# Kernel tuning notes

Hardware: AMD Instinct MI355X
Metric: run time of the kernel (lower is better)

The kernel has to match this reference:

```python
import jax, jax.numpy as jnp
import numpy as np

N = 100000      # nodes
E = 1600000     # edges (avg degree 16)
D_IN, D_H, D_OUT = 100, 256, 47
EPS = 1e-5


def setup_inputs() -> dict:
    key = jax.random.key(0)
    ks = jax.random.split(key, 10)
    w = lambda k, s: jax.random.normal(k, s, jnp.float32) * 0.02
    return {
        "x": jax.random.normal(ks[0], (N, D_IN), jnp.float32),
        "edge_index": jax.random.randint(ks[1], (2, E), 0, N),
        # SAGEConv 0: lin_l (aggregated neighbors, has bias), lin_r (root, no bias)
        "wl0": w(ks[2], (D_IN, D_H)), "wr0": w(ks[3], (D_IN, D_H)), "b0": jnp.zeros((D_H,), jnp.float32),
        "g0": jnp.ones((D_H,), jnp.float32), "be0": jnp.zeros((D_H,), jnp.float32),
        # SAGEConv 1
        "wl1": w(ks[4], (D_H, D_H)), "wr1": w(ks[5], (D_H, D_H)), "b1": jnp.zeros((D_H,), jnp.float32),
        "g1": jnp.ones((D_H,), jnp.float32), "be1": jnp.zeros((D_H,), jnp.float32),
        # SAGEConv 2 (output)
        "wl2": w(ks[6], (D_H, D_OUT)), "wr2": w(ks[7], (D_H, D_OUT)), "b2": jnp.zeros((D_OUT,), jnp.float32),
    }


def _sage_conv(x, src, dst, wl, wr, b):
    # mean aggregation of source-node features onto destination nodes
    agg = jax.ops.segment_sum(x[src], dst, num_segments=N)          # [N, d_in]
    cnt = jax.ops.segment_sum(jnp.ones((src.shape[0],), x.dtype), dst, num_segments=N)
    mean = agg / jnp.maximum(cnt, 1.0)[:, None]                     # 0 in-degree -> 0
    return mean @ wl + x @ wr + b


def _bn(h, gamma, beta):
    m = h.mean(axis=0)
    v = h.var(axis=0)
    return (h - m) * jax.lax.rsqrt(v + EPS) * gamma + beta


def reference(x, edge_index, wl0, wr0, b0, g0, be0, wl1, wr1, b1, g1, be1, wl2, wr2, b2):
    src, dst = edge_index[0], edge_index[1]
    h = jax.nn.relu(_bn(_sage_conv(x, src, dst, wl0, wr0, b0), g0, be0))
    h = jax.nn.relu(_bn(_sage_conv(h, src, dst, wl1, wr1, b1), g1, be1))
    h = _sage_conv(h, src, dst, wl2, wr2, b2)
    return jax.nn.log_softmax(h, axis=1)
```

## Files before the change

kernel.cpp:

```cpp
#include <hip/hip_runtime.h>
#include <hip/hip_bf16.h>
#include <math.h>

#define DEVFN __device__ __forceinline__

typedef unsigned int uint32;
typedef unsigned short ushort_t;

using bf16x8 = __attribute__((ext_vector_type(8))) short;
using f32x4  = __attribute__((ext_vector_type(4))) float;

DEVFN float bf2f(ushort_t u) {
    union { uint32 i; float f; } v; v.i = ((uint32)u) << 16; return v.f;
}
DEVFN ushort_t f2bf(float f) {
    union { float f; uint32 i; } v; v.f = f;
    uint32 u = v.i;
    uint32 r = (u + 0x7FFFu + ((u >> 16) & 1u)) >> 16;
    return (ushort_t)r;
}

DEVFN void gload_lds16(const void* g, void* l) {
    __builtin_amdgcn_global_load_lds(
        (const __attribute__((address_space(1))) void*)g,
        (__attribute__((address_space(3))) void*)l, 16, 0, 0);
}

__global__ void k_cast_x(const float* __restrict__ x, ushort_t* __restrict__ xb, int N) {
    int total = N * 128;
    for (int i = blockIdx.x * blockDim.x + threadIdx.x; i < total; i += gridDim.x * blockDim.x) {
        int col = i & 127, row = i >> 7;
        float v = (col < 100) ? x[row * 100 + col] : 0.f;
        xb[i] = f2bf(v);
    }
}

__global__ void k_cast_w(const float* __restrict__ w, ushort_t* __restrict__ wt,
                         int K, int Nout, int Kp, int Np) {
    int total = Np * Kp;
    for (int i = blockIdx.x * blockDim.x + threadIdx.x; i < total; i += gridDim.x * blockDim.x) {
        int k = i % Kp, n = i / Kp;
        float v = (k < K && n < Nout) ? w[k * Nout + n] : 0.f;
        wt[i] = f2bf(v);
    }
}

__global__ void k_bincount(const int* __restrict__ dst, int E, int CH, int nbins, int nblk,
                           int* __restrict__ binCnt) {
    __shared__ int scnt[128];
    int blk = blockIdx.x, tid = threadIdx.x;
    for (int b = tid; b < 128; b += 256) scnt[b] = 0;
    __syncthreads();
    int e0 = blk * CH, e1 = min(E, e0 + CH);
    for (int i = e0 + tid; i < e1; i += 256)
        atomicAdd(&scnt[dst[i] >> 10], 1);
    __syncthreads();
    for (int b = tid; b < nbins; b += 256) binCnt[b * nblk + blk] = scnt[b];
}

__global__ void k_blocksum(const int* __restrict__ v, int n, int* __restrict__ bsum) {
    __shared__ int s[1024];
    int i = blockIdx.x * 1024 + threadIdx.x;
    s[threadIdx.x] = (i < n) ? v[i] : 0;
    __syncthreads();
    for (int o = 512; o > 0; o >>= 1) {
        if (threadIdx.x < o) s[threadIdx.x] += s[threadIdx.x + o];
        __syncthreads();
    }
    if (threadIdx.x == 0) bsum[blockIdx.x] = s[0];
}

__global__ void k_scanb(int* __restrict__ bsum, int NB) {
    if (blockIdx.x == 0 && threadIdx.x == 0) {
        int acc = 0;
        for (int i = 0; i < NB; ++i) { int v = bsum[i]; bsum[i] = acc; acc += v; }
    }
}

__global__ void k_exscan(const int* __restrict__ v, const int* __restrict__ bsum,
                         int n, int* __restrict__ outOff) {
    __shared__ int s[1024];
    int t = threadIdx.x;
    int i = blockIdx.x * 1024 + t;
    int val = (i < n) ? v[i] : 0;
    s[t] = val;
    __syncthreads();
    for (int o = 1; o < 1024; o <<= 1) {
        int add = (t >= o) ? s[t - o] : 0;
        __syncthreads();
        s[t] += add;
        __syncthreads();
    }
    if (i < n) outOff[i] = s[t] - val + bsum[blockIdx.x];
}

__global__ void k_binscatter(const int* __restrict__ src, const int* __restrict__ dst,
                             int E, int CH, int nbins, int nblk,
                             const int* __restrict__ binOff, int* __restrict__ ebin) {
    __shared__ int scur[128];
    int blk = blockIdx.x, tid = threadIdx.x;
    for (int b = tid; b < nbins; b += 256) scur[b] = binOff[b * nblk + blk];
    __syncthreads();
    int e0 = blk * CH, e1 = min(E, e0 + CH);
    for (int i = e0 + tid; i < e1; i += 256) {
        int d = dst[i];
        int b = d >> 10;
        int pos = atomicAdd(&scur[b], 1);
        ebin[pos] = (src[i] << 10) | (d & 1023);
    }
}

__global__ void k_bincsr(const int* __restrict__ ebin, const int* __restrict__ binOff,
                         int E, int N, int nbins, int nblk,
                         int* __restrict__ offs, int* __restrict__ deg, int* __restrict__ csr) {
    __shared__ int sdeg[1024];
    __shared__ int scur[1024];
    int bin = blockIdx.x, t = threadIdx.x;
    int binStart = binOff[bin * nblk];
    int binEnd = (bin + 1 < nbins) ? binOff[(bin + 1) * nblk] : E;
    sdeg[t] = 0;
    __syncthreads();
    for (int i = binStart + t; i < binEnd; i += 1024)
        atomicAdd(&sdeg[ebin[i] & 1023], 1);
    __syncthreads();
    int v = sdeg[t];
    for (int o = 1; o < 1024; o <<= 1) {
        int add = (t >= o) ? sdeg[t - o] : 0;
        __syncthreads();
        sdeg[t] += add;
        __syncthreads();
    }
    int ex = sdeg[t] - v;
    int node = bin * 1024 + t;
    if (node < N) { offs[node] = binStart + ex; deg[node] = v; }
    scur[t] = ex;
    __syncthreads();
    for (int i = binStart + t; i < binEnd; i += 1024) {
        int e = ebin[i];
        int slot = atomicAdd(&scur[e & 1023], 1);
        csr[binStart + slot] = e >> 10;
    }
}

template <int DIMS>
__global__ void k_agg(const ushort_t* __restrict__ h, const int* __restrict__ offs,
                      const int* __restrict__ deg, const int* __restrict__ csr,
                      int N, ushort_t* __restrict__ mean) {
    constexpr int VPL = DIMS / 64;
    int wid = (blockIdx.x * blockDim.x + threadIdx.x) >> 6;
    int lane = threadIdx.x & 63;
    if (wid >= N) return;
    int off = offs[wid], cnt = deg[wid];
    float acc[VPL] = {};
    const ushort_t* hp = h + (size_t)lane * VPL;
    int j = 0;
    if constexpr (VPL == 2) {
        for (; j + 8 <= cnt; j += 8) {
            int s[8];
#pragma unroll
            for (int u = 0; u < 8; ++u) s[u] = csr[off + j + u];
            uint32 d[8];
#pragma unroll
            for (int u = 0; u < 8; ++u) d[u] = *(const uint32*)(hp + (size_t)s[u] * DIMS);
#pragma unroll
            for (int u = 0; u < 8; ++u) {
                acc[0] += bf2f((ushort_t)(d[u] & 0xffff));
                acc[1] += bf2f((ushort_t)(d[u] >> 16));
            }
        }
        for (; j < cnt; ++j) {
            uint32 u = *(const uint32*)(hp + (size_t)csr[off + j] * DIMS);
            acc[0] += bf2f((ushort_t)(u & 0xffff));
            acc[1] += bf2f((ushort_t)(u >> 16));
        }
    } else {
        for (; j + 8 <= cnt; j += 8) {
            int s[8];
#pragma unroll
            for (int u = 0; u < 8; ++u) s[u] = csr[off + j + u];
            uint2 d[8];
#pragma unroll
            for (int u = 0; u < 8; ++u) d[u] = *(const uint2*)(hp + (size_t)s[u] * DIMS);
#pragma unroll
            for (int u = 0; u < 8; ++u) {
                acc[0] += bf2f((ushort_t)(d[u].x & 0xffff));
                acc[1] += bf2f((ushort_t)(d[u].x >> 16));
                acc[2] += bf2f((ushort_t)(d[u].y & 0xffff));
                acc[3] += bf2f((ushort_t)(d[u].y >> 16));
            }
        }
        for (; j < cnt; ++j) {
            uint2 u = *(const uint2*)(hp + (size_t)csr[off + j] * DIMS);
            acc[0] += bf2f((ushort_t)(u.x & 0xffff));
            acc[1] += bf2f((ushort_t)(u.x >> 16));
            acc[2] += bf2f((ushort_t)(u.y & 0xffff));
            acc[3] += bf2f((ushort_t)(u.y >> 16));
        }
    }
    float inv = 1.f / fmaxf((float)cnt, 1.f);
    if constexpr (VPL == 2) {
        uint32 o = (uint32)f2bf(acc[0] * inv) | ((uint32)f2bf(acc[1] * inv) << 16);
        *(uint32*)(mean + (size_t)wid * DIMS + lane * 2) = o;
    } else {
        uint2 o;
        o.x = (uint32)f2bf(acc[0] * inv) | ((uint32)f2bf(acc[1] * inv) << 16);
        o.y = (uint32)f2bf(acc[2] * inv) | ((uint32)f2bf(acc[3] * inv) << 16);
        *(uint2*)(mean + (size_t)wid * DIMS + lane * 4) = o;
    }
}

template <int BN, int WAVES_N, int WM, int WN, int MODE>
__global__ __launch_bounds__(256) void k_gemm(
    const ushort_t* __restrict__ A1, const ushort_t* __restrict__ B1,
    const ushort_t* __restrict__ A2, const ushort_t* __restrict__ B2,
    int KP, const float* __restrict__ bias,
    ushort_t* __restrict__ out_bf, float* __restrict__ out_f,
    float* __restrict__ stats, int M) {
    constexpr int BM = 128, BK = 32;
    constexpr int M_REP = WM / 16, N_REP = WN / 16;
    constexpr int SIDES = (MODE == 0) ? 2 : 1;
    __shared__ ushort_t Alds[BM * BK];
    __shared__ ushort_t Blds[BN * BK];
    __shared__ float sstat[2][BN];
    const int tid = threadIdx.x, lane = tid & 63, wid = tid >> 6;
    const int wm = wid / WAVES_N, wn = wid % WAVES_N;
    const int row0 = blockIdx.x * BM, col0 = blockIdx.y * BN;
    if (MODE == 0) {
        for (int i = tid; i < 2 * BN; i += 256) (&sstat[0][0])[i] = 0.f;
    }
    f32x4 acc[M_REP][N_REP] = {};
    for (int side = 0; side < SIDES; ++side) {
        const ushort_t* A = side ? A2 : A1;
        const ushort_t* B = side ? B2 : B1;
        for (int kt = 0; kt < KP; kt += BK) {
            __syncthreads();
            for (int i = tid; i < BM * 4; i += 256) {
                int r = i >> 2, c = i & 3;
                int gr = row0 + r;
                if (gr >= M) gr = M - 1;
                gload_lds16(A + (size_t)gr * KP + kt + c * 8, Alds + i * 8);
            }
            for (int i = tid; i < BN * 4; i += 256) {
                int r = i >> 2, c = i & 3;
                gload_lds16(B + (size_t)(col0 + r) * KP + kt + c * 8, Blds + i * 8);
            }
            __syncthreads();
            bf16x8 a[M_REP], b[N_REP];
#pragma unroll
            for (int m = 0; m < M_REP; ++m)
                a[m] = *(const bf16x8*)&Alds[(wm * WM + m * 16 + (lane & 15)) * BK + (lane >> 4) * 8];
#pragma unroll
            for (int n = 0; n < N_REP; ++n)
                b[n] = *(const bf16x8*)&Blds[(wn * WN + n * 16 + (lane & 15)) * BK + (lane >> 4) * 8];
#pragma unroll
            for (int m = 0; m < M_REP; ++m)
#pragma unroll
                for (int n = 0; n < N_REP; ++n)
                    acc[m][n] = __builtin_amdgcn_mfma_f32_16x16x32_bf16(a[m], b[n], acc[m][n], 0, 0, 0);
        }
    }
#pragma unroll
    for (int n = 0; n < N_REP; ++n) {
        int lcol = wn * WN + n * 16 + (lane & 15);
        float s = 0.f, q = 0.f;
#pragma unroll
        for (int m = 0; m < M_REP; ++m) {
#pragma unroll
            for (int r = 0; r < 4; ++r) {
                int row = row0 + wm * WM + m * 16 + (lane >> 4) * 4 + r;
                float v = acc[m][n][r];
                if (row < M) {
                    if (MODE == 0) {
                        out_bf[(size_t)row * 256 + col0 + lcol] = f2bf(v);
                        s += v;
                        q += v * v;
                    } else {
                        if (lcol < 64) {
                            out_bf[(size_t)row * 64 + lcol] = f2bf(v);
                        } else {
                            int c = lcol - 64;
                            float bv = (c < 47) ? bias[c] : 0.f;
                            out_f[(size_t)row * 64 + c] = v + bv;
                        }
                    }
                }
            }
        }
        if (MODE == 0) {
            s += __shfl_xor(s, 16); s += __shfl_xor(s, 32);
            q += __shfl_xor(q, 16); q += __shfl_xor(q, 32);
            if (lane < 16) {
                atomicAdd(&sstat[0][lcol], s);
                atomicAdd(&sstat[1][lcol], q);
            }
        }
    }
    if (MODE == 0) {
        __syncthreads();
        for (int i = tid; i < BN; i += 256) {
            atomicAdd(&stats[col0 + i], sstat[0][i]);
            atomicAdd(&stats[256 + col0 + i], sstat[1][i]);
        }
    }
}

__global__ void k_bnrelu(const ushort_t* __restrict__ h, const float* __restrict__ stats,
                         const float* __restrict__ g, const float* __restrict__ be,
                         int M, ushort_t* __restrict__ out) {
    int c = threadIdx.x;
    float invM = 1.f / (float)M;
    float mean = stats[c] * invM;
    float var = stats[256 + c] * invM - mean * mean;
    float sc = g[c] * rsqrtf(var + 1e-5f);
    float sh = be[c] - mean * sc;
    for (int r = blockIdx.x; r < M; r += gridDim.x) {
        float v = bf2f(h[(size_t)r * 256 + c]) * sc + sh;
        out[(size_t)r * 256 + c] = f2bf(fmaxf(v, 0.f));
    }
}

__global__ void k_agg_lsm(const ushort_t* __restrict__ t2, const float* __restrict__ r2,
                          const int* __restrict__ offs, const int* __restrict__ deg,
                          const int* __restrict__ csr, int N, float* __restrict__ out) {
    int wid = (blockIdx.x * blockDim.x + threadIdx.x) >> 6;
    int lane = threadIdx.x & 63;
    if (wid >= N) return;
    int off = offs[wid], cnt = deg[wid];
    float acc = 0.f;
    const ushort_t* tp = t2 + lane;
    int j = 0;
    for (; j + 8 <= cnt; j += 8) {
        int s[8];
#pragma unroll
        for (int u = 0; u < 8; ++u) s[u] = csr[off + j + u];
        ushort_t d[8];
#pragma unroll
        for (int u = 0; u < 8; ++u) d[u] = tp[(size_t)s[u] * 64];
#pragma unroll
        for (int u = 0; u < 8; ++u) acc += bf2f(d[u]);
    }
    for (; j < cnt; ++j) acc += bf2f(tp[(size_t)csr[off + j] * 64]);
    float v = acc / fmaxf((float)cnt, 1.f) + r2[(size_t)wid * 64 + lane];
    if (lane >= 47) v = -1e30f;
    float m = v;
    for (int o = 32; o > 0; o >>= 1) m = fmaxf(m, __shfl_xor(m, o));
    float e = (lane < 47) ? expf(v - m) : 0.f;
    float sum = e;
    for (int o = 32; o > 0; o >>= 1) sum += __shfl_xor(sum, o);
    if (lane < 47) out[(size_t)wid * 47 + lane] = v - m - logf(sum);
}

extern "C" void kernel_launch(void* const* d_in, const int* in_sizes, int n_in,
                              void* d_out, int out_size, void* d_ws, size_t ws_size,
                              hipStream_t stream) {
    const float* x   = (const float*)d_in[0];
    const int*   ei  = (const int*)d_in[1];
    const float* wl0 = (const float*)d_in[2];
    const float* wr0 = (const float*)d_in[3];
    const float* g0  = (const float*)d_in[5];
    const float* be0 = (const float*)d_in[6];
    const float* wl1 = (const float*)d_in[7];
    const float* wr1 = (const float*)d_in[8];
    const float* g1  = (const float*)d_in[10];
    const float* be1 = (const float*)d_in[11];
    const float* wl2 = (const float*)d_in[12];
    const float* wr2 = (const float*)d_in[13];
    const float* b2  = (const float*)d_in[14];
    float* out = (float*)d_out;

    const int N = in_sizes[0] / 100;
    const int E = in_sizes[1] / 2;
    const int* src = ei;
    const int* dst = ei + E;

    char* p = (char*)d_ws;
    auto alloc = [&](size_t bytes) -> char* {
        char* r = p;
        p += (bytes + 255) & ~(size_t)255;
        return r;
    };
    ushort_t* xb   = (ushort_t*)alloc((size_t)N * 128 * 2);
    ushort_t* hbuf = (ushort_t*)alloc((size_t)N * 256 * 2);
    ushort_t* mean = (ushort_t*)alloc((size_t)N * 256 * 2);
    ushort_t* hpre = (ushort_t*)alloc((size_t)N * 256 * 2);
    int* deg  = (int*)alloc((size_t)N * 4);
    int* offs = (int*)alloc((size_t)N * 4);
    int* csr  = (int*)alloc((size_t)E * 4);
    int* ebin = (int*)alloc((size_t)E * 4);
    const int NBLK = 128;
    const int nbins = (N + 1023) >> 10;
    const int scanN = nbins * NBLK;
    int* binCnt = (int*)alloc((size_t)scanN * 4);
    int* binOff = (int*)alloc((size_t)scanN * 4);
    int* bsum = (int*)alloc(1024 * 4);
    float* stats = (float*)alloc(512 * 4);
    ushort_t* wlt0 = (ushort_t*)alloc(256 * 128 * 2);
    ushort_t* wrt0 = (ushort_t*)alloc(256 * 128 * 2);
    ushort_t* wlt1 = (ushort_t*)alloc(256 * 256 * 2);
    ushort_t* wrt1 = (ushort_t*)alloc(256 * 256 * 2);
    ushort_t* wcat2 = (ushort_t*)alloc(128 * 256 * 2);
    if ((size_t)(p - (char*)d_ws) > ws_size) return;

    ushort_t* t2 = mean;
    float*    r2 = (float*)((char*)mean + (size_t)N * 64 * 2);

    k_cast_x<<<2048, 256, 0, stream>>>(x, xb, N);
    k_cast_w<<<128, 256, 0, stream>>>(wl0, wlt0, 100, 256, 128, 256);
    k_cast_w<<<128, 256, 0, stream>>>(wr0, wrt0, 100, 256, 128, 256);
    k_cast_w<<<128, 256, 0, stream>>>(wl1, wlt1, 256, 256, 256, 256);
    k_cast_w<<<128, 256, 0, stream>>>(wr1, wrt1, 256, 256, 256, 256);
    k_cast_w<<<128, 256, 0, stream>>>(wl2, wcat2, 256, 47, 256, 64);
    k_cast_w<<<128, 256, 0, stream>>>(wr2, wcat2 + 64 * 256, 256, 47, 256, 64);

    const int CH = (E + NBLK - 1) / NBLK;
    k_bincount<<<NBLK, 256, 0, stream>>>(dst, E, CH, nbins, NBLK, binCnt);
    int NB2 = (scanN + 1023) / 1024;
    k_blocksum<<<NB2, 1024, 0, stream>>>(binCnt, scanN, bsum);
    k_scanb<<<1, 64, 0, stream>>>(bsum, NB2);
    k_exscan<<<NB2, 1024, 0, stream>>>(binCnt, bsum, scanN, binOff);
    k_binscatter<<<NBLK, 256, 0, stream>>>(src, dst, E, CH, nbins, NBLK, binOff, ebin);
    k_bincsr<<<nbins, 1024, 0, stream>>>(ebin, binOff, E, N, nbins, NBLK, offs, deg, csr);

    int aggBlocks = (N + 3) / 4;
    int gemmM = (N + 127) / 128;

    k_agg<128><<<aggBlocks, 256, 0, stream>>>(xb, offs, deg, csr, N, mean);
    hipMemsetAsync(stats, 0, 512 * 4, stream);
    k_gemm<128, 2, 64, 64, 0><<<dim3(gemmM, 2), 256, 0, stream>>>(
        mean, wlt0, xb, wrt0, 128, nullptr, hpre, nullptr, stats, N);
    k_bnrelu<<<2048, 256, 0, stream>>>(hpre, stats, g0, be0, N, hbuf);

    k_agg<256><<<aggBlocks, 256, 0, stream>>>(hbuf, offs, deg, csr, N, mean);
    hipMemsetAsync(stats, 0, 512 * 4, stream);
    k_gemm<128, 2, 64, 64, 0><<<dim3(gemmM, 2), 256, 0, stream>>>(
        mean, wlt1, hbuf, wrt1, 256, nullptr, hpre, nullptr, stats, N);
    k_bnrelu<<<2048, 256, 0, stream>>>(hpre, stats, g1, be1, N, hbuf);

    k_gemm<128, 2, 64, 64, 1><<<dim3(gemmM, 1), 256, 0, stream>>>(
        hbuf, wcat2, nullptr, nullptr, 256, b2, t2, r2, nullptr, N);
    k_agg_lsm<<<(N + 3) / 4, 256, 0, stream>>>(t2, r2, offs, deg, csr, N, out);
}
```

Baseline: 600.0 us.

## Prefetch neighbor indices in aggregation and widen GEMM tiles to full width

The aggregation kernels now prefetch the next batch of CSR indices while the current feature gathers are in flight. Tails are handled by clamped indices and a zero weight instead of a scalar remainder loop, and the batch size is set per feature width. The GEMM now uses 512 threads, a K-tile of 64, and one block covering all 256 (or 128) output columns. This removes the second column-block pass that re-read the A operand and halves the number of barriers per K. The cost is more LDS and registers per block, which may lower occupancy, plus extra wasted gathers for low-degree nodes.

```diff
diff --git a/kernel.cpp b/kernel.cpp
--- a/kernel.cpp
+++ b/kernel.cpp
@@ -142,7 +142,7 @@
     }
 }
 
-template <int DIMS>
+template <int DIMS, int BATCH>
 __global__ void k_agg(const ushort_t* __restrict__ h, const int* __restrict__ offs,
                       const int* __restrict__ deg, const int* __restrict__ csr,
                       int N, ushort_t* __restrict__ mean) {
@@ -153,48 +153,42 @@
     int off = offs[wid], cnt = deg[wid];
     float acc[VPL] = {};
     const ushort_t* hp = h + (size_t)lane * VPL;
-    int j = 0;
-    if constexpr (VPL == 2) {
-        for (; j + 8 <= cnt; j += 8) {
-            int s[8];
-#pragma unroll
-            for (int u = 0; u < 8; ++u) s[u] = csr[off + j + u];
-            uint32 d[8];
-#pragma unroll
-            for (int u = 0; u < 8; ++u) d[u] = *(const uint32*)(hp + (size_t)s[u] * DIMS);
-#pragma unroll
-            for (int u = 0; u < 8; ++u) {
-                acc[0] += bf2f((ushort_t)(d[u] & 0xffff));
-                acc[1] += bf2f((ushort_t)(d[u] >> 16));
-            }
-        }
-        for (; j < cnt; ++j) {
-            uint32 u = *(const uint32*)(hp + (size_t)csr[off + j] * DIMS);
-            acc[0] += bf2f((ushort_t)(u & 0xffff));
-            acc[1] += bf2f((ushort_t)(u >> 16));
-        }
-    } else {
-        for (; j + 8 <= cnt; j += 8) {
-            int s[8];
-#pragma unroll
-            for (int u = 0; u < 8; ++u) s[u] = csr[off + j + u];
-            uint2 d[8];
-#pragma unroll
-            for (int u = 0; u < 8; ++u) d[u] = *(const uint2*)(hp + (size_t)s[u] * DIMS);
-#pragma unroll
-            for (int u = 0; u < 8; ++u) {
-                acc[0] += bf2f((ushort_t)(d[u].x & 0xffff));
-                acc[1] += bf2f((ushort_t)(d[u].x >> 16));
-                acc[2] += bf2f((ushort_t)(d[u].y & 0xffff));
-                acc[3] += bf2f((ushort_t)(d[u].y >> 16));
-            }
-        }
-        for (; j < cnt; ++j) {
-            uint2 u = *(const uint2*)(hp + (size_t)csr[off + j] * DIMS);
-            acc[0] += bf2f((ushort_t)(u.x & 0xffff));
-            acc[1] += bf2f((ushort_t)(u.x >> 16));
-            acc[2] += bf2f((ushort_t)(u.y & 0xffff));
-            acc[3] += bf2f((ushort_t)(u.y >> 16));
+    if (cnt > 0) {
+        int idx[BATCH];
+#pragma unroll
+        for (int u = 0; u < BATCH; ++u) idx[u] = csr[off + min(u, cnt - 1)];
+        for (int b = 0; b < cnt; b += BATCH) {
+            if constexpr (VPL == 2) {
+                uint32 d[BATCH];
+#pragma unroll
+                for (int u = 0; u < BATCH; ++u)
+                    d[u] = *(const uint32*)(hp + (size_t)idx[u] * DIMS);
+                int nxt = b + BATCH;
+#pragma unroll
+                for (int u = 0; u < BATCH; ++u) idx[u] = csr[off + min(nxt + u, cnt - 1)];
+#pragma unroll
+                for (int u = 0; u < BATCH; ++u) {
+                    float w = (b + u < cnt) ? 1.f : 0.f;
+                    acc[0] += w * bf2f((ushort_t)(d[u] & 0xffff));
+                    acc[1] += w * bf2f((ushort_t)(d[u] >> 16));
+                }
+            } else {
+                uint2 d[BATCH];
+#pragma unroll
+                for (int u = 0; u < BATCH; ++u)
+                    d[u] = *(const uint2*)(hp + (size_t)idx[u] * DIMS);
+                int nxt = b + BATCH;
+#pragma unroll
+                for (int u = 0; u < BATCH; ++u) idx[u] = csr[off + min(nxt + u, cnt - 1)];
+#pragma unroll
+                for (int u = 0; u < BATCH; ++u) {
+                    float w = (b + u < cnt) ? 1.f : 0.f;
+                    acc[0] += w * bf2f((ushort_t)(d[u].x & 0xffff));
+                    acc[1] += w * bf2f((ushort_t)(d[u].x >> 16));
+                    acc[2] += w * bf2f((ushort_t)(d[u].y & 0xffff));
+                    acc[3] += w * bf2f((ushort_t)(d[u].y >> 16));
+                }
+            }
         }
     }
     float inv = 1.f / fmaxf((float)cnt, 1.f);
@@ -209,24 +203,25 @@
     }
 }
 
-template <int BN, int WAVES_N, int WM, int WN, int MODE>
-__global__ __launch_bounds__(256) void k_gemm(
+template <int BN, int WROWS, int WCOLS, int MODE>
+__global__ __launch_bounds__(512) void k_gemm(
     const ushort_t* __restrict__ A1, const ushort_t* __restrict__ B1,
     const ushort_t* __restrict__ A2, const ushort_t* __restrict__ B2,
     int KP, const float* __restrict__ bias,
     ushort_t* __restrict__ out_bf, float* __restrict__ out_f,
     float* __restrict__ stats, int M) {
-    constexpr int BM = 128, BK = 32;
+    constexpr int BM = 128, BK = 64;
+    constexpr int WM = BM / WROWS, WN = BN / WCOLS;
     constexpr int M_REP = WM / 16, N_REP = WN / 16;
     constexpr int SIDES = (MODE == 0) ? 2 : 1;
     __shared__ ushort_t Alds[BM * BK];
     __shared__ ushort_t Blds[BN * BK];
     __shared__ float sstat[2][BN];
     const int tid = threadIdx.x, lane = tid & 63, wid = tid >> 6;
-    const int wm = wid / WAVES_N, wn = wid % WAVES_N;
-    const int row0 = blockIdx.x * BM, col0 = blockIdx.y * BN;
+    const int wm = wid / WCOLS, wn = wid % WCOLS;
+    const int row0 = blockIdx.x * BM;
     if (MODE == 0) {
-        for (int i = tid; i < 2 * BN; i += 256) (&sstat[0][0])[i] = 0.f;
+        for (int i = tid; i < 2 * BN; i += 512) (&sstat[0][0])[i] = 0.f;
     }
     f32x4 acc[M_REP][N_REP] = {};
     for (int side = 0; side < SIDES; ++side) {
@@ -234,29 +229,36 @@
         const ushort_t* B = side ? B2 : B1;
         for (int kt = 0; kt < KP; kt += BK) {
             __syncthreads();
-            for (int i = tid; i < BM * 4; i += 256) {
-                int r = i >> 2, c = i & 3;
+#pragma unroll
+            for (int i = tid; i < BM * BK / 8; i += 512) {
+                int r = i >> 3, c = i & 7;
                 int gr = row0 + r;
                 if (gr >= M) gr = M - 1;
                 gload_lds16(A + (size_t)gr * KP + kt + c * 8, Alds + i * 8);
             }
-            for (int i = tid; i < BN * 4; i += 256) {
-                int r = i >> 2, c = i & 3;
-                gload_lds16(B + (size_t)(col0 + r) * KP + kt + c * 8, Blds + i * 8);
+#pragma unroll
+            for (int i = tid; i < BN * BK / 8; i += 512) {
+                int r = i >> 3, c = i & 7;
+                gload_lds16(B + (size_t)r * KP + kt + c * 8, Blds + i * 8);
             }
             __syncthreads();
-            bf16x8 a[M_REP], b[N_REP];
-#pragma unroll
-            for (int m = 0; m < M_REP; ++m)
-                a[m] = *(const bf16x8*)&Alds[(wm * WM + m * 16 + (lane & 15)) * BK + (lane >> 4) * 8];
-#pragma unroll
-            for (int n = 0; n < N_REP; ++n)
-                b[n] = *(const bf16x8*)&Blds[(wn * WN + n * 16 + (lane & 15)) * BK + (lane >> 4) * 8];
-#pragma unroll
-            for (int m = 0; m < M_REP; ++m)
+            bf16x8 a[2][M_REP], b[2][N_REP];
+#pragma unroll
+            for (int kk = 0; kk < 2; ++kk) {
+#pragma unroll
+                for (int m = 0; m < M_REP; ++m)
+                    a[kk][m] = *(const bf16x8*)&Alds[(wm * WM + m * 16 + (lane & 15)) * BK + kk * 32 + (lane >> 4) * 8];
 #pragma unroll
                 for (int n = 0; n < N_REP; ++n)
-                    acc[m][n] = __builtin_amdgcn_mfma_f32_16x16x32_bf16(a[m], b[n], acc[m][n], 0, 0, 0);
+                    b[kk][n] = *(const bf16x8*)&Blds[(wn * WN + n * 16 + (lane & 15)) * BK + kk * 32 + (lane >> 4) * 8];
+            }
+#pragma unroll
+            for (int kk = 0; kk < 2; ++kk)
+#pragma unroll
+                for (int m = 0; m < M_REP; ++m)
+#pragma unroll
+                    for (int n = 0; n < N_REP; ++n)
+                        acc[m][n] = __builtin_amdgcn_mfma_f32_16x16x32_bf16(a[kk][m], b[kk][n], acc[m][n], 0, 0, 0);
         }
     }
 #pragma unroll
@@ -271,7 +273,7 @@
                 float v = acc[m][n][r];
                 if (row < M) {
                     if (MODE == 0) {
-                        out_bf[(size_t)row * 256 + col0 + lcol] = f2bf(v);
+                        out_bf[(size_t)row * 256 + lcol] = f2bf(v);
                         s += v;
                         q += v * v;
                     } else {
@@ -297,9 +299,9 @@
     }
     if (MODE == 0) {
         __syncthreads();
-        for (int i = tid; i < BN; i += 256) {
-            atomicAdd(&stats[col0 + i], sstat[0][i]);
-            atomicAdd(&stats[256 + col0 + i], sstat[1][i]);
+        for (int i = tid; i < BN; i += 512) {
+            atomicAdd(&stats[i], sstat[0][i]);
+            atomicAdd(&stats[256 + i], sstat[1][i]);
         }
     }
 }
@@ -322,24 +324,31 @@
 __global__ void k_agg_lsm(const ushort_t* __restrict__ t2, const float* __restrict__ r2,
                           const int* __restrict__ offs, const int* __restrict__ deg,
                           const int* __restrict__ csr, int N, float* __restrict__ out) {
+    constexpr int BATCH = 16;
     int wid = (blockIdx.x * blockDim.x + threadIdx.x) >> 6;
     int lane = threadIdx.x & 63;
     if (wid >= N) return;
     int off = offs[wid], cnt = deg[wid];
     float acc = 0.f;
     const ushort_t* tp = t2 + lane;
-    int j = 0;
-    for (; j + 8 <= cnt; j += 8) {
-        int s[8];
-#pragma unroll
-        for (int u = 0; u < 8; ++u) s[u] = csr[off + j + u];
-        ushort_t d[8];
-#pragma unroll
-        for (int u = 0; u < 8; ++u) d[u] = tp[(size_t)s[u] * 64];
-#pragma unroll
-        for (int u = 0; u < 8; ++u) acc += bf2f(d[u]);
-    }
-    for (; j < cnt; ++j) acc += bf2f(tp[(size_t)csr[off + j] * 64]);
+    if (cnt > 0) {
+        int idx[BATCH];
+#pragma unroll
+        for (int u = 0; u < BATCH; ++u) idx[u] = csr[off + min(u, cnt - 1)];
+        for (int b = 0; b < cnt; b += BATCH) {
+            ushort_t d[BATCH];
+#pragma unroll
+            for (int u = 0; u < BATCH; ++u) d[u] = tp[(size_t)idx[u] * 64];
+            int nxt = b + BATCH;
+#pragma unroll
+            for (int u = 0; u < BATCH; ++u) idx[u] = csr[off + min(nxt + u, cnt - 1)];
+#pragma unroll
+            for (int u = 0; u < BATCH; ++u) {
+                float w = (b + u < cnt) ? 1.f : 0.f;
+                acc += w * bf2f(d[u]);
+            }
+        }
+    }
     float v = acc / fmaxf((float)cnt, 1.f) + r2[(size_t)wid * 64 + lane];
     if (lane >= 47) v = -1e30f;
     float m = v;
@@ -424,19 +433,19 @@
     int aggBlocks = (N + 3) / 4;
     int gemmM = (N + 127) / 128;
 
-    k_agg<128><<<aggBlocks, 256, 0, stream>>>(xb, offs, deg, csr, N, mean);
+    k_agg<128, 16><<<aggBlocks, 256, 0, stream>>>(xb, offs, deg, csr, N, mean);
     hipMemsetAsync(stats, 0, 512 * 4, stream);
-    k_gemm<128, 2, 64, 64, 0><<<dim3(gemmM, 2), 256, 0, stream>>>(
+    k_gemm<256, 2, 4, 0><<<gemmM, 512, 0, stream>>>(
         mean, wlt0, xb, wrt0, 128, nullptr, hpre, nullptr, stats, N);
     k_bnrelu<<<2048, 256, 0, stream>>>(hpre, stats, g0, be0, N, hbuf);
 
-    k_agg<256><<<aggBlocks, 256, 0, stream>>>(hbuf, offs, deg, csr, N, mean);
+    k_agg<256, 8><<<aggBlocks, 256, 0, stream>>>(hbuf, offs, deg, csr, N, mean);
     hipMemsetAsync(stats, 0, 512 * 4, stream);
-    k_gemm<128, 2, 64, 64, 0><<<dim3(gemmM, 2), 256, 0, stream>>>(
+    k_gemm<256, 2, 4, 0><<<gemmM, 512, 0, stream>>>(
         mean, wlt1, hbuf, wrt1, 256, nullptr, hpre, nullptr, stats, N);
     k_bnrelu<<<2048, 256, 0, stream>>>(hpre, stats, g1, be1, N, hbuf);
 
-    k_gemm<128, 2, 64, 64, 1><<<dim3(gemmM, 1), 256, 0, stream>>>(
+    k_gemm<128, 2, 4, 1><<<gemmM, 512, 0, stream>>>(
         hbuf, wcat2, nullptr, nullptr, 256, b2, t2, r2, nullptr, N);
     k_agg_lsm<<<(N + 3) / 4, 256, 0, stream>>>(t2, r2, offs, deg, csr, N, out);
 }
```

New measurement: 580.9 us. 3.2% less time.
